# Kernel optimization log

Hardware: AMD Instinct MI355X
Metric: run time of the kernel (lower is better)

## Reference

```python
import jax, jax.numpy as jnp
import numpy as np

B, S, I, H, O = 256, 2048, 32, 128, 1


def setup_inputs() -> dict:
    key = jax.random.key(0)
    ks = jax.random.split(key, 9)
    sI = 1.0 / np.sqrt(I)
    sH = 1.0 / np.sqrt(H)
    sD = 1.0 / np.sqrt(H * S)
    return {
        "x": jax.random.normal(ks[0], (B, S, I), jnp.float32),
        "Wi": jax.random.normal(ks[1], (I, H), jnp.float32) * sI,
        "bi": jax.random.normal(ks[2], (H,), jnp.float32) * sI,
        "Wh": jax.random.normal(ks[3], (H, H), jnp.float32) * sH,
        "bh": jax.random.normal(ks[4], (H,), jnp.float32) * sH,
        "Wa": jax.random.normal(ks[5], (H, 1), jnp.float32) * sH,
        "ba": jax.random.normal(ks[6], (1,), jnp.float32) * sH,
        "Wd": jax.random.normal(ks[7], (H * S, O), jnp.float32) * sD,
        "bd": jax.random.normal(ks[8], (O,), jnp.float32) * sD,
        "resDepth": 4,
    }


def _branch_ids(seq_len: int, resDepth: int) -> np.ndarray:
    # Encodes the per-step branch of ResRNN_Cell.forward (static in i, resDepth):
    # 0: i==0 (set hstart, h0 stays zero)   1: i==lag-2 -> h0=tanh(hn+hstart)
    # 4: resDepth==1 -> h0=tanh(hn+h0)      2: i%resDepth==0 -> h0=tanh(hn+ht), ht=hn
    # 3: else -> h0=tanh(hn)
    br = np.full(seq_len, 3, dtype=np.int32)
    br[(np.arange(seq_len) % resDepth) == 0] = 2
    if resDepth == 1:
        br[:] = 4
    br[seq_len - 2] = 1
    br[0] = 0
    return br


def reference(x, Wi, bi, Wh, bh, Wa, ba, Wd, bd, resDepth):
    batch, seq_len, _ = x.shape
    hid = Wh.shape[0]
    br = _branch_ids(seq_len, int(resDepth))
    f0, f1, f2, f4 = (jnp.asarray(br == k) for k in (0, 1, 2, 4))
    xs = jnp.swapaxes(x, 0, 1)  # (S, B, I)
    z = jnp.zeros((batch, hid), x.dtype)

    def step(carry, inp):
        h0, ht, hstart = carry
        xt, g0, g1, g2, g4 = inp
        hn = xt @ Wi + bi + h0 @ Wh + bh  # (B, H)
        hstart = jnp.where(g0, hn, hstart)
        cand = jnp.where(g1, jnp.tanh(hn + hstart),
               jnp.where(g4, jnp.tanh(hn + h0),
               jnp.where(g2, jnp.tanh(hn + ht), jnp.tanh(hn))))
        h0n = jnp.where(g0, h0, cand)  # at i==0 h0 is NOT updated in the original
        htn = jnp.where(g2, hn, ht)
        return (h0n, htn, hstart), hn

    _, hiddens = jax.lax.scan(step, (z, z, z), (xs, f0, f1, f2, f4))
    # hiddens: (S, B, H) == torch.cat(outputs, 0)
    scores = hiddens @ Wa + ba  # (S, B, 1)
    # faithful to the original's .view((batchSize, -1)) on (S,B,1)-contiguous data
    att = jax.nn.softmax(scores.reshape(batch, seq_len), axis=-1)
    att = att.reshape(seq_len, batch, 1)
    weighted = hiddens * att  # (S, B, H)
    # faithful to .view(-1, hiddenNum * seq_len) on (S,B,H)-contiguous data
    flat = weighted.reshape(batch, seq_len * hid)
    return flat @ Wd + bd
```

## Files before the change

### kernel.cpp

```cpp
#include <hip/hip_runtime.h>
#include <math.h>

#define B_ 256
#define S_ 2048
#define I_ 32
#define H_ 128

typedef float v2f __attribute__((ext_vector_type(2)));
__device__ __forceinline__ v2f mk2(float a, float b) { v2f r; r.x = a; r.y = b; return r; }

__device__ __forceinline__ void pk_fma_lo(v2f& d, v2f a, v2f b) {
    asm("v_pk_fma_f32 %0, %1, %2, %0 op_sel:[0,0,0] op_sel_hi:[0,1,1]"
        : "+v"(d) : "v"(a), "v"(b));
}
__device__ __forceinline__ void pk_fma_hi(v2f& d, v2f a, v2f b) {
    asm("v_pk_fma_f32 %0, %1, %2, %0 op_sel:[1,0,0] op_sel_hi:[1,1,1]"
        : "+v"(d) : "v"(a), "v"(b));
}

__device__ __forceinline__ void sync_lds() {
    asm volatile("" ::: "memory");
    asm volatile("s_waitcnt lgkmcnt(0)" ::: "memory");
    __builtin_amdgcn_s_barrier();
    asm volatile("" ::: "memory");
}

__device__ __forceinline__ float fast_tanh(float z) {
    float e = __expf(2.0f * z);
    return 1.0f - 2.0f / (e + 1.0f);
}

template <int CTRL>
__device__ __forceinline__ float dppf(float v) {
    return __int_as_float(__builtin_amdgcn_update_dpp(
        0, __float_as_int(v), CTRL, 0xF, 0xF, false));
}

__device__ __forceinline__ float swz_xor16(float v) {
    return __int_as_float(__builtin_amdgcn_ds_swizzle(__float_as_int(v), 0x401F));
}

#define CHP 12

#define PKD(hv, base)                                             \
    pk_fma_lo(acc01, mk2((hv).x, (hv).y), W01[(base) + 0]);       \
    pk_fma_lo(acc23, mk2((hv).x, (hv).y), W23[(base) + 0]);       \
    pk_fma_hi(acc01, mk2((hv).x, (hv).y), W01[(base) + 1]);       \
    pk_fma_hi(acc23, mk2((hv).x, (hv).y), W23[(base) + 1]);       \
    pk_fma_lo(acc01, mk2((hv).z, (hv).w), W01[(base) + 2]);       \
    pk_fma_lo(acc23, mk2((hv).z, (hv).w), W23[(base) + 2]);       \
    pk_fma_hi(acc01, mk2((hv).z, (hv).w), W01[(base) + 3]);       \
    pk_fma_hi(acc23, mk2((hv).z, (hv).w), W23[(base) + 3]);

#define UP_REDUCE(RING)                                                       \
    {                                                                         \
      float r = uP;                                                           \
      r += dppf<0xB1>(r);                                                     \
      r += dppf<0x4E>(r);                                                     \
      if ((l & 0xB) == 0)                                                     \
        ((float*)&pl_lds[RING][(w << 2) | ((l >> 4) & 3)])[(l >> 2) & 1] = r; \
    }

#define PL_COMBINE(RING, SIDX)                                                \
    {                                                                         \
      float2 pp = pl_lds[RING][l & 31];                                       \
      float px = pp.x, py = pp.y;                                             \
      px += dppf<0xB1>(px);  py += dppf<0xB1>(py);                            \
      px += dppf<0x4E>(px);  py += dppf<0x4E>(py);                            \
      px += dppf<0x141>(px); py += dppf<0x141>(py);                           \
      px += dppf<0x128>(px); py += dppf<0x128>(py);                           \
      px += swz_xor16(px);   py += swz_xor16(py);                             \
      if (l == 0) part[((SIDX) << 8) + b] = make_float2(px, py);              \
    }

#define MAT_CORE(XS)                                                          \
    v2f acc01 = bias01, acc23 = bias23;                                       \
    pk_fma_lo(acc01, mk2((XS).x, (XS).y), WiF01[0]);                          \
    pk_fma_hi(acc01, mk2((XS).x, (XS).y), WiF01[1]);                          \
    pk_fma_lo(acc23, mk2((XS).x, (XS).y), WiF23[0]);                          \
    pk_fma_hi(acc23, mk2((XS).x, (XS).y), WiF23[1]);                          \
    PKD(hvA, 0) PKD(hvB, 4)                                                   \
    float p0 = acc01.x + dppf<0x141>(acc01.x);                                \
    float p1 = acc01.y + dppf<0x141>(acc01.y);                                \
    float p2 = acc23.x + dppf<0x141>(acc23.x);                                \
    float p3 = acc23.y + dppf<0x141>(acc23.y);                                \
    float s01x = p0 + dppf<0xB1>(p0);                                         \
    float s01y = p1 + dppf<0xB1>(p1);                                         \
    float s23x = p2 + dppf<0xB1>(p2);                                         \
    float s23y = p3 + dppf<0xB1>(p3);                                         \
    float t0 = kb0 ? s01y : s01x;                                             \
    float t1 = kb0 ? s23y : s23x;                                             \
    t0 += dppf<0x4E>(t0);                                                     \
    t1 += dppf<0x4E>(t1);                                                     \
    float tt = kb1 ? t1 : t0;                                                 \
    tt += dppf<0x128>(tt);                                                    \
    const float hn = tt;

#define STEP_FULL(g, PH, XS, CPH)                                             \
  {                                                                           \
    const int s_ = (g) * 8 + (PH);                                            \
    const float* hb = &h0_lds[(PH) & 1][0];                                   \
    float4 hvA = *(const float4*)(hb + rdoff);                                \
    float4 hvB = *(const float4*)(hb + rdoff + 4);                            \
    if (s_ >= 1) UP_REDUCE(((PH) + 3) & 3)                                    \
    if (w == (PH) && s_ >= 2) PL_COMBINE(((PH) + 2) & 3, s_ - 2)              \
    MAT_CORE(XS)                                                              \
    if (s_ < S_ - 2) {                                                        \
      (XS) = *(const float2*)(xgrp + ((PH) + 2) * I_);                        \
    }                                                                         \
    uP = hn * (CPH);                                                          \
    float h0n;                                                                \
    if (s_ == 0)            { hstartR = hn; h0n = 0.0f; }                     \
    else if (s_ == S_ - 2)  { h0n = fast_tanh(hn + hstartR); }                \
    else if (rd == 1)       { h0n = fast_tanh(hn + h0R); }                    \
    else if (cnt == 0)      { h0n = fast_tanh(hn + htR); htR = hn; }          \
    else                    { h0n = fast_tanh(hn); }                          \
    h0R = h0n;                                                                \
    if (wmask) h0_lds[((PH) + 1) & 1][hwoff] = h0n;                           \
    cnt = (cnt + 1 == rd) ? 0 : cnt + 1;                                      \
    sync_lds();                                                               \
  }

#define STEP_LEAN4(g, PH, XS, CPH)                                            \
  {                                                                           \
    const float* hb = &h0_lds[(PH) & 1][0];                                   \
    float4 hvA = *(const float4*)(hb + rdoff);                                \
    float4 hvB = *(const float4*)(hb + rdoff + 4);                            \
    UP_REDUCE(((PH) + 3) & 3)                                                 \
    if (w == (PH)) PL_COMBINE(((PH) + 2) & 3, (g) * 8 + (PH) - 2)             \
    MAT_CORE(XS)                                                              \
    (XS) = *(const float2*)(xgrp + ((PH) + 2) * I_);                          \
    uP = hn * (CPH);                                                          \
    float h0n;                                                                \
    if (((PH) & 3) == 0) { h0n = fast_tanh(hn + htR); htR = hn; }             \
    else                 { h0n = fast_tanh(hn); }                             \
    if (wmask) h0_lds[((PH) + 1) & 1][hwoff] = h0n;                           \
    sync_lds();                                                               \
  }

#define STEP_LEAN(g, PH, XS, CPH)                                             \
  {                                                                           \
    const float* hb = &h0_lds[(PH) & 1][0];                                   \
    float4 hvA = *(const float4*)(hb + rdoff);                                \
    float4 hvB = *(const float4*)(hb + rdoff + 4);                            \
    UP_REDUCE(((PH) + 3) & 3)                                                 \
    if (w == (PH)) PL_COMBINE(((PH) + 2) & 3, (g) * 8 + (PH) - 2)             \
    MAT_CORE(XS)                                                              \
    (XS) = *(const float2*)(xgrp + ((PH) + 2) * I_);                          \
    uP = hn * (CPH);                                                          \
    const bool c0 = (cnt == 0);                                               \
    float resid = rd1 ? h0R : (c0 ? htR : 0.0f);                              \
    float h0n = fast_tanh(hn + resid);                                        \
    htR = (htup && c0) ? hn : htR;                                            \
    h0R = h0n;                                                                \
    if (wmask) h0_lds[((PH) + 1) & 1][hwoff] = h0n;                           \
    cnt = (cnt + 1 == rd) ? 0 : cnt + 1;                                      \
    sync_lds();                                                               \
  }

__global__ __launch_bounds__(512)
__attribute__((amdgpu_waves_per_eu(2, 2)))
void rnn_kernel(
    const float* __restrict__ x, const float* __restrict__ Wi,
    const float* __restrict__ bi, const float* __restrict__ Wh,
    const float* __restrict__ bh, const float* __restrict__ Wa,
    const float* __restrict__ Wd, const int* __restrict__ rdp,
    float2* __restrict__ part)
{
    const int b = blockIdx.x;
    const int t = threadIdx.x;
    const int w = t >> 6;
    const int l = t & 63;
    const int  kg4   = l & 15;
    const int  hg2   = (l >> 4) & 3;
    const int  hbase = 16 * w + 4 * hg2;
    const int  hf    = hbase + (l & 3);
    const bool kb0   = (l & 1);
    const bool kb1   = (l >> 1) & 1;
    const bool wmask = ((l & 0xC) == 0);
    const int  rdoff = kg4 * CHP;
    const int  hwoff = (hf >> 3) * CHP + (hf & 7);

    __shared__ __align__(16) float h0_lds[2][16 * CHP];
    __shared__ __align__(8)  float2 pl_lds[4][32];

    const int rd = rdp[0];
    const bool rd1  = (rd == 1);
    const bool htup = !rd1;
    if (t < 16 * CHP) h0_lds[0][t] = 0.0f;

    v2f W01[8], W23[8];
#pragma unroll
    for (int c = 0; c < 8; ++c) {
        int k = 8 * kg4 + c;
        float4 q = *(const float4*)(Wh + (size_t)k * H_ + hbase);
        W01[c] = mk2(q.x, q.y);
        W23[c] = mk2(q.z, q.w);
    }
    const int i0 = 2 * kg4;
    v2f WiF01[2], WiF23[2];
#pragma unroll
    for (int j = 0; j < 2; ++j) {
        float2 a = *(const float2*)(Wi + (size_t)(i0 + j) * H_ + hbase);
        float2 c = *(const float2*)(Wi + (size_t)(i0 + j) * H_ + hbase + 2);
        WiF01[j] = mk2(a.x, a.y);
        WiF23[j] = mk2(c.x, c.y);
    }
    const bool k0g = (kg4 == 0);
    const v2f bias01 = k0g ? mk2(bi[hbase] + bh[hbase],
                                 bi[hbase + 1] + bh[hbase + 1]) : mk2(0.f, 0.f);
    const v2f bias23 = k0g ? mk2(bi[hbase + 2] + bh[hbase + 2],
                                 bi[hbase + 3] + bh[hbase + 3]) : mk2(0.f, 0.f);

    const bool clsq = (l >> 2) & 1;
    const float waC = Wa[hf];
    float cph[8];
#pragma unroll
    for (int K = 0; K < 8; ++K)
        cph[K] = clsq ? Wd[(K << 15) + (b << 7) + hf] : waC;

    const float* xgrp = x + (size_t)b * (S_ * I_) + i0;
    float2 xS0 = *(const float2*)xgrp;
    float2 xS1 = *(const float2*)(xgrp + I_);

    sync_lds();

    float htR = 0.f, hstartR = 0.f, h0R = 0.f;
    float uP = 0.f;
    int cnt = 0;

    {
        STEP_FULL(0, 0, xS0, cph[0])
        STEP_FULL(0, 1, xS1, cph[1])
        STEP_FULL(0, 2, xS0, cph[2])
        STEP_FULL(0, 3, xS1, cph[3])
        STEP_FULL(0, 4, xS0, cph[4])
        STEP_FULL(0, 5, xS1, cph[5])
        STEP_FULL(0, 6, xS0, cph[6])
        STEP_FULL(0, 7, xS1, cph[7])
        xgrp += 8 * I_;
    }
    if (rd == 4) {
        for (int g = 1; g < 255; ++g) {
            STEP_LEAN4(g, 0, xS0, cph[0])
            STEP_LEAN4(g, 1, xS1, cph[1])
            STEP_LEAN4(g, 2, xS0, cph[2])
            STEP_LEAN4(g, 3, xS1, cph[3])
            STEP_LEAN4(g, 4, xS0, cph[4])
            STEP_LEAN4(g, 5, xS1, cph[5])
            STEP_LEAN4(g, 6, xS0, cph[6])
            STEP_LEAN4(g, 7, xS1, cph[7])
            xgrp += 8 * I_;
        }
        cnt = 0;
    } else {
        for (int g = 1; g < 255; ++g) {
            STEP_LEAN(g, 0, xS0, cph[0])
            STEP_LEAN(g, 1, xS1, cph[1])
            STEP_LEAN(g, 2, xS0, cph[2])
            STEP_LEAN(g, 3, xS1, cph[3])
            STEP_LEAN(g, 4, xS0, cph[4])
            STEP_LEAN(g, 5, xS1, cph[5])
            STEP_LEAN(g, 6, xS0, cph[6])
            STEP_LEAN(g, 7, xS1, cph[7])
            xgrp += 8 * I_;
        }
    }
    {
        STEP_FULL(255, 0, xS0, cph[0])
        STEP_FULL(255, 1, xS1, cph[1])
        STEP_FULL(255, 2, xS0, cph[2])
        STEP_FULL(255, 3, xS1, cph[3])
        STEP_FULL(255, 4, xS0, cph[4])
        STEP_FULL(255, 5, xS1, cph[5])
        STEP_FULL(255, 6, xS0, cph[6])
        STEP_FULL(255, 7, xS1, cph[7])
    }

    UP_REDUCE(3)
    sync_lds();
    if (w == 0) PL_COMBINE(2, S_ - 2)
    if (w == 1) PL_COMBINE(3, S_ - 1)
}

__global__ __launch_bounds__(256) void attn_kernel(
    const float2* __restrict__ part, const float* __restrict__ bd,
    float* __restrict__ out)
{
    const int r = blockIdx.x;
    const int t = threadIdx.x;
    float sc[8], dv[8];
    float mx = -1e30f;
#pragma unroll
    for (int u = 0; u < 8; ++u) {
        int f = (r << 11) + (u << 8) + t;
        float2 a = part[f];
        sc[u] = a.x;
        dv[u] = a.y;
        mx = fmaxf(mx, sc[u]);
    }
    __shared__ float redm[4], redz[4], redw[4];
#pragma unroll
    for (int off = 32; off > 0; off >>= 1) mx = fmaxf(mx, __shfl_xor(mx, off, 64));
    if ((t & 63) == 0) redm[t >> 6] = mx;
    __syncthreads();
    mx = fmaxf(fmaxf(redm[0], redm[1]), fmaxf(redm[2], redm[3]));
    float z = 0.f, wv = 0.f;
#pragma unroll
    for (int u = 0; u < 8; ++u) {
        float e = __expf(sc[u] - mx);
        z += e;
        wv += e * dv[u];
    }
#pragma unroll
    for (int off = 32; off > 0; off >>= 1) {
        z += __shfl_xor(z, off, 64);
        wv += __shfl_xor(wv, off, 64);
    }
    if ((t & 63) == 0) { redz[t >> 6] = z; redw[t >> 6] = wv; }
    __syncthreads();
    if (t == 0) {
        float Z = redz[0] + redz[1] + redz[2] + redz[3];
        float W = redw[0] + redw[1] + redw[2] + redw[3];
        out[r] = bd[0] + W / Z;
    }
}

extern "C" void kernel_launch(void* const* d_in, const int* in_sizes, int n_in,
                              void* d_out, int out_size, void* d_ws, size_t ws_size,
                              hipStream_t stream) {
    const float* x  = (const float*)d_in[0];
    const float* Wi = (const float*)d_in[1];
    const float* bi = (const float*)d_in[2];
    const float* Wh = (const float*)d_in[3];
    const float* bh = (const float*)d_in[4];
    const float* Wa = (const float*)d_in[5];
    const float* Wd = (const float*)d_in[7];
    const float* bd = (const float*)d_in[8];
    const int*  rdp = (const int*)d_in[9];

    float2* part = (float2*)d_ws;

    rnn_kernel<<<B_, 512, 0, stream>>>(x, Wi, bi, Wh, bh, Wa, Wd, rdp, part);
    attn_kernel<<<B_, 256, 0, stream>>>(part, bd, (float*)d_out);
}
```

Before: 863.1 us.

## Pack two batch rows per 1024-thread workgroup in the RNN kernel

New measurement: 1.328 ms. 53.8% more time.

```diff
diff --git a/kernel.cpp b/kernel.cpp
--- a/kernel.cpp
+++ b/kernel.cpp
@@ -5,6 +5,7 @@
 #define S_ 2048
 #define I_ 32
 #define H_ 128
+#define BPB 2
 
 typedef float v2f __attribute__((ext_vector_type(2)));
 __device__ __forceinline__ v2f mk2(float a, float b) { v2f r; r.x = a; r.y = b; return r; }
@@ -58,12 +59,12 @@
       r += dppf<0xB1>(r);                                                     \
       r += dppf<0x4E>(r);                                                     \
       if ((l & 0xB) == 0)                                                     \
-        ((float*)&pl_lds[RING][(w << 2) | ((l >> 4) & 3)])[(l >> 2) & 1] = r; \
+        ((float*)&pl_lds[bb][RING][(w << 2) | ((l >> 4) & 3)])[(l >> 2) & 1] = r; \
     }
 
 #define PL_COMBINE(RING, SIDX)                                                \
     {                                                                         \
-      float2 pp = pl_lds[RING][l & 31];                                       \
+      float2 pp = pl_lds[bb][RING][l & 31];                                   \
       float px = pp.x, py = pp.y;                                             \
       px += dppf<0xB1>(px);  py += dppf<0xB1>(py);                            \
       px += dppf<0x4E>(px);  py += dppf<0x4E>(py);                            \
@@ -99,7 +100,7 @@
 #define STEP_FULL(g, PH, XS, CPH)                                             \
   {                                                                           \
     const int s_ = (g) * 8 + (PH);                                            \
-    const float* hb = &h0_lds[(PH) & 1][0];                                   \
+    const float* hb = &h0_lds[bb][(PH) & 1][0];                               \
     float4 hvA = *(const float4*)(hb + rdoff);                                \
     float4 hvB = *(const float4*)(hb + rdoff + 4);                            \
     if (s_ >= 1) UP_REDUCE(((PH) + 3) & 3)                                    \
@@ -116,14 +117,14 @@
     else if (cnt == 0)      { h0n = fast_tanh(hn + htR); htR = hn; }          \
     else                    { h0n = fast_tanh(hn); }                          \
     h0R = h0n;                                                                \
-    if (wmask) h0_lds[((PH) + 1) & 1][hwoff] = h0n;                           \
+    if (wmask) h0_lds[bb][((PH) + 1) & 1][hwoff] = h0n;                       \
     cnt = (cnt + 1 == rd) ? 0 : cnt + 1;                                      \
     sync_lds();                                                               \
   }
 
 #define STEP_LEAN4(g, PH, XS, CPH)                                            \
   {                                                                           \
-    const float* hb = &h0_lds[(PH) & 1][0];                                   \
+    const float* hb = &h0_lds[bb][(PH) & 1][0];                               \
     float4 hvA = *(const float4*)(hb + rdoff);                                \
     float4 hvB = *(const float4*)(hb + rdoff + 4);                            \
     UP_REDUCE(((PH) + 3) & 3)                                                 \
@@ -134,13 +135,13 @@
     float h0n;                                                                \
     if (((PH) & 3) == 0) { h0n = fast_tanh(hn + htR); htR = hn; }             \
     else                 { h0n = fast_tanh(hn); }                             \
-    if (wmask) h0_lds[((PH) + 1) & 1][hwoff] = h0n;                           \
+    if (wmask) h0_lds[bb][((PH) + 1) & 1][hwoff] = h0n;                       \
     sync_lds();                                                               \
   }
 
 #define STEP_LEAN(g, PH, XS, CPH)                                             \
   {                                                                           \
-    const float* hb = &h0_lds[(PH) & 1][0];                                   \
+    const float* hb = &h0_lds[bb][(PH) & 1][0];                               \
     float4 hvA = *(const float4*)(hb + rdoff);                                \
     float4 hvB = *(const float4*)(hb + rdoff + 4);                            \
     UP_REDUCE(((PH) + 3) & 3)                                                 \
@@ -153,13 +154,12 @@
     float h0n = fast_tanh(hn + resid);                                        \
     htR = (htup && c0) ? hn : htR;                                            \
     h0R = h0n;                                                                \
-    if (wmask) h0_lds[((PH) + 1) & 1][hwoff] = h0n;                           \
+    if (wmask) h0_lds[bb][((PH) + 1) & 1][hwoff] = h0n;                       \
     cnt = (cnt + 1 == rd) ? 0 : cnt + 1;                                      \
     sync_lds();                                                               \
   }
 
-__global__ __launch_bounds__(512)
-__attribute__((amdgpu_waves_per_eu(2, 2)))
+__global__ __launch_bounds__(1024)
 void rnn_kernel(
     const float* __restrict__ x, const float* __restrict__ Wi,
     const float* __restrict__ bi, const float* __restrict__ Wh,
@@ -167,10 +167,12 @@
     const float* __restrict__ Wd, const int* __restrict__ rdp,
     float2* __restrict__ part)
 {
-    const int b = blockIdx.x;
     const int t = threadIdx.x;
-    const int w = t >> 6;
-    const int l = t & 63;
+    const int w16 = t >> 6;
+    const int bb  = w16 >> 3;
+    const int w   = w16 & 7;
+    const int b   = blockIdx.x * BPB + bb;
+    const int l   = t & 63;
     const int  kg4   = l & 15;
     const int  hg2   = (l >> 4) & 3;
     const int  hbase = 16 * w + 4 * hg2;
@@ -181,13 +183,13 @@
     const int  rdoff = kg4 * CHP;
     const int  hwoff = (hf >> 3) * CHP + (hf & 7);
 
-    __shared__ __align__(16) float h0_lds[2][16 * CHP];
-    __shared__ __align__(8)  float2 pl_lds[4][32];
+    __shared__ __align__(16) float h0_lds[BPB][2][16 * CHP];
+    __shared__ __align__(8)  float2 pl_lds[BPB][4][32];
 
     const int rd = rdp[0];
     const bool rd1  = (rd == 1);
     const bool htup = !rd1;
-    if (t < 16 * CHP) h0_lds[0][t] = 0.0f;
+    if (t < BPB * 16 * CHP) h0_lds[t / (16 * CHP)][0][t % (16 * CHP)] = 0.0f;
 
     v2f W01[8], W23[8];
 #pragma unroll
@@ -341,6 +343,6 @@
 
     float2* part = (float2*)d_ws;
 
-    rnn_kernel<<<B_, 512, 0, stream>>>(x, Wi, bi, Wh, bh, Wa, Wd, rdp, part);
+    rnn_kernel<<<B_ / BPB, 1024, 0, stream>>>(x, Wi, bi, Wh, bh, Wa, Wd, rdp, part);
     attn_kernel<<<B_, 256, 0, stream>>>(part, bd, (float*)d_out);
 }
```
